# Optimization experiments

Hardware: AMD Instinct MI355X
Metric: run time of the kernel (lower is better)

The kernel has to match this reference:

```python
import jax, jax.numpy as jnp
import numpy as np

N = 16384   # total queries (= total keys here)
B = 16      # scenes
K = 1024    # keys per scene (key_batch_cnt entries)
L = 32      # local neighborhood size
D = 256     # d_model
H = 8       # nhead
DFF = 1024
LN_EPS = 1e-5


def setup_inputs() -> dict:
    key = jax.random.key(0)
    ks = jax.random.split(key, 32)
    f32 = jnp.float32

    def lin(k, o, i):
        return jax.random.normal(k, (o, i), f32) * 0.02

    idx = jax.random.randint(ks[3], (N, L), 0, K)
    invalid = jax.random.uniform(ks[4], (N, L)) < 0.1
    index_pair = jnp.where(invalid, -1, idx).astype(jnp.int32)

    inp = {
        "tgt": jax.random.normal(ks[0], (N, D), f32),
        "memory": jax.random.normal(ks[1], (N, D), f32),
        "memory_pos_emb": jax.random.normal(ks[2], (N, D), f32),
        "key_batch_cnt": jnp.full((B,), K, dtype=jnp.int32),
        "index_pair": index_pair,
        "index_pair_batch": jnp.repeat(jnp.arange(B, dtype=jnp.int32), K),
        "Wq": lin(ks[5], D, D), "bq": jnp.zeros((D,), f32),
        "Wkc": lin(ks[6], D, D), "bkc": jnp.zeros((D,), f32),
        "Wkp": lin(ks[7], D, D), "bkp": jnp.zeros((D,), f32),
        "Wv": lin(ks[8], D, D), "bv": jnp.zeros((D,), f32),
        "Wo": lin(ks[9], D, D), "bo": jnp.zeros((D,), f32),
        "W1": lin(ks[10], DFF, D), "b1": jnp.zeros((DFF,), f32),
        "W2": lin(ks[11], D, DFF), "b2": jnp.zeros((D,), f32),
        "g2": jnp.ones((D,), f32), "be2": jnp.zeros((D,), f32),
        "g3": jnp.ones((D,), f32), "be3": jnp.zeros((D,), f32),
    }
    return inp


def _ln(x, g, b):
    m = jnp.mean(x, axis=-1, keepdims=True)
    v = jnp.mean((x - m) ** 2, axis=-1, keepdims=True)
    return (x - m) * jax.lax.rsqrt(v + LN_EPS) * g + b


def reference(tgt, memory, memory_pos_emb, key_batch_cnt, index_pair,
              index_pair_batch, Wq, bq, Wkc, bkc, Wkp, bkp, Wv, bv,
              Wo, bo, W1, b1, W2, b2, g2, be2, g3, be3):
    Dh = D // H
    scale = Dh ** -0.5

    # dense projections
    q = tgt @ Wq.T + bq                              # [N, D]
    k = (memory @ Wkc.T + bkc) + (memory_pos_emb @ Wkp.T + bkp)  # content + pos
    v = memory @ Wv.T + bv

    # local-index gather: per-batch indices -> global key indices
    offsets = jnp.concatenate([jnp.zeros((1,), jnp.int32),
                               jnp.cumsum(key_batch_cnt)[:-1].astype(jnp.int32)])
    mask = index_pair < 0                            # [N, L] padded neighbors
    gidx = jnp.where(mask, 0, index_pair + offsets[index_pair_batch][:, None])

    kg = k[gidx].reshape(N, L, H, Dh)                # gathered keys  [N,L,H,Dh]
    vg = v[gidx].reshape(N, L, H, Dh)                # gathered values
    qh = q.reshape(N, H, Dh)

    attn = jnp.einsum('nhd,nlhd->nhl', qh, kg) * scale
    attn = jnp.where(mask[:, None, :], -1e9, attn)
    attn = jax.nn.softmax(attn, axis=-1)
    out = jnp.einsum('nhl,nlhd->nhd', attn, vg).reshape(N, D)
    tgt2 = out @ Wo.T + bo                           # attention out_proj

    x = _ln(tgt + tgt2, g2, be2)
    ff = jax.nn.relu(x @ W1.T + b1) @ W2.T + b2
    return _ln(x + ff, g3, be3)
```

## Files before the change

### kernel.cpp

```cpp
#include <hip/hip_runtime.h>
#include <stdint.h>

#define N_TOT 16384
#define LNEI  32
#define DM    256
#define NH    8
#define DH    32
#define DFF   1024

typedef __attribute__((ext_vector_type(8))) short  short8;
typedef __attribute__((ext_vector_type(4))) float  floatx4;
typedef __attribute__((ext_vector_type(2))) float  float2_t;
typedef __attribute__((ext_vector_type(4))) int    intx4;
typedef __attribute__((ext_vector_type(4))) unsigned short ushort4_t;
typedef __attribute__((ext_vector_type(4))) unsigned int uint4_t;

static __device__ __forceinline__ float b2f(unsigned short u) {
  union { unsigned int u; float f; } x; x.u = ((unsigned int)u) << 16; return x.f;
}
static __device__ __forceinline__ unsigned short f2b(float f) {
  union { float f; unsigned int u; } x; x.f = f;
  unsigned int r = x.u + 0x7fffu + ((x.u >> 16) & 1u);
  return (unsigned short)(r >> 16);
}

#define NSEG 11
struct Seg { const float* src; unsigned short* dst; int cols; int ostride; int ooff; int begin; };
struct SegTable { Seg s[NSEG]; int total; };

__global__ __launch_bounds__(256) void cvt_all(SegTable T, float* biaskv,
                                               const float* bkc, const float* bkp,
                                               const float* bv) {
  int e = (blockIdx.x * 256 + threadIdx.x) * 4;
  if (e >= T.total) {
    int c = e - T.total;
    #pragma unroll
    for (int j = 0; j < 4; ++j, ++c)
      if (c < 512) biaskv[c] = (c < 256) ? (bkc[c] + bkp[c]) : bv[c - 256];
    return;
  }
  int si = 0;
  #pragma unroll
  for (int i = 1; i < NSEG; ++i) if (e >= T.s[i].begin) si = i;
  const Seg s = T.s[si];
  const int le = e - s.begin;
  const int row = le / s.cols;
  const int col = le - row * s.cols;
  floatx4 v = {0.f, 0.f, 0.f, 0.f};
  if (s.src) v = *(const floatx4*)(s.src + le);
  ushort4_t o;
  o.x = f2b(v[0]); o.y = f2b(v[1]); o.z = f2b(v[2]); o.w = f2b(v[3]);
  *(ushort4_t*)(s.dst + (size_t)row * s.ostride + s.ooff + col) = o;
}

static __device__ __forceinline__ void gl_lds16(const unsigned short* g, unsigned short* l) {
  __builtin_amdgcn_global_load_lds(
      (const __attribute__((address_space(1))) unsigned int*)g,
      (__attribute__((address_space(3))) unsigned int*)l, 16, 0, 0);
}

template<int BN, bool RELU, bool CF32>
__global__ __launch_bounds__(256) void gemm_tile(
    const unsigned short* __restrict__ A, const unsigned short* __restrict__ W,
    const float* __restrict__ bias,
    void* __restrict__ C, int M, int Nd, int K, int lda)
{
  constexpr int BM = 128, BK = 32;
  constexpr int MI = (BN == 128) ? 4 : 2;
  constexpr int NI = 4;
  __shared__ unsigned short sA[2][BM * BK];
  __shared__ unsigned short sB[2][BN * BK];

  const int w    = threadIdx.x >> 6;
  const int lane = threadIdx.x & 63;
  const int quad = lane >> 4;
  const int l16  = lane & 15;
  const int m0 = blockIdx.x * BM;
  const int n0 = blockIdx.y * BN;
  const int wrow0 = (BN == 128) ? (w >> 1) * 64 : w * 32;
  const int wcol0 = (BN == 128) ? (w & 1) * 64 : 0;

  const int aflat0 = w * 512 + lane * 8;
  const int ar0 = aflat0 >> 5, ac = aflat0 & 31;

  floatx4 acc[MI][NI] = {};

  for (int k0 = 0; k0 < K; k0 += 2 * BK) {
    __syncthreads();
    #pragma unroll
    for (int half = 0; half < 2; ++half) {
      const int kk = k0 + half * BK;
      #pragma unroll
      for (int c = 0; c < 2; ++c) {
        const int row = ar0 + c * 64;
        gl_lds16(A + (size_t)(m0 + row) * lda + kk + ac, &sA[half][(c * 4 + w) * 512]);
      }
      if (BN == 128) {
        #pragma unroll
        for (int c = 0; c < 2; ++c) {
          const int row = ar0 + c * 64;
          gl_lds16(W + (size_t)(n0 + row) * K + kk + ac, &sB[half][(c * 4 + w) * 512]);
        }
      } else {
        gl_lds16(W + (size_t)(n0 + ar0) * K + kk + ac, &sB[half][w * 512]);
      }
    }
    __syncthreads();

    #pragma unroll
    for (int half = 0; half < 2; ++half) {
      short8 af[MI], bf[NI];
      #pragma unroll
      for (int mi = 0; mi < MI; ++mi)
        af[mi] = *(const short8*)&sA[half][(wrow0 + mi * 16 + l16) * BK + quad * 8];
      #pragma unroll
      for (int ni = 0; ni < NI; ++ni)
        bf[ni] = *(const short8*)&sB[half][(wcol0 + ni * 16 + l16) * BK + quad * 8];
      #pragma unroll
      for (int mi = 0; mi < MI; ++mi)
        #pragma unroll
        for (int ni = 0; ni < NI; ++ni)
          acc[mi][ni] = __builtin_amdgcn_mfma_f32_16x16x32_bf16(af[mi], bf[ni], acc[mi][ni], 0, 0, 0);
    }
  }

  #pragma unroll
  for (int ni = 0; ni < NI; ++ni) {
    const int col = n0 + wcol0 + ni * 16 + l16;
    const float bvv = bias[col];
    #pragma unroll
    for (int mi = 0; mi < MI; ++mi) {
      const int row0 = m0 + wrow0 + mi * 16 + quad * 4;
      #pragma unroll
      for (int i = 0; i < 4; ++i) {
        float v = acc[mi][ni][i] + bvv;
        if (RELU) v = fmaxf(v, 0.f);
        if (CF32) ((float*)C)[(size_t)(row0 + i) * Nd + col] = v;
        else ((unsigned short*)C)[(size_t)(row0 + i) * Nd + col] = f2b(v);
      }
    }
  }
}

__global__ __launch_bounds__(256) void attn_kernel(
    const unsigned short* __restrict__ q, const float* __restrict__ kv,
    const int* __restrict__ key_batch_cnt, const int* __restrict__ index_pair,
    const int* __restrict__ index_pair_batch,
    unsigned short* __restrict__ out)
{
  const int n = ((blockIdx.x & 7) << 11) | (blockIdx.x >> 3);
  const int t = threadIdx.x;
  __shared__ float s_q[DM];
  __shared__ int   s_gidx[LNEI];
  __shared__ float s_score[NH][LNEI];
  __shared__ float s_prob[NH][LNEI];
  __shared__ float s_out[2][DM];

  s_q[t] = b2f(q[(size_t)n * DM + t]);
  if (t < 64) {
    const int b = index_pair_batch[n];
    int cnt = (t < 16) ? key_batch_cnt[t] : 0;
    cnt = (t < b) ? cnt : 0;
    #pragma unroll
    for (int msk = 32; msk >= 1; msk >>= 1) cnt += __shfl_xor(cnt, msk, 64);
    if (t < LNEI) {
      const int ip = index_pair[(size_t)n * LNEI + t];
      s_gidx[t] = (ip < 0) ? -1 : (ip + cnt);
    }
  }
  __syncthreads();

  {
    const int j  = t >> 3;
    const int c8 = t & 7;
    const int g  = s_gidx[j];
    const int gl = (g < 0) ? 0 : g;
    const float* kbase = kv + (size_t)gl * 512;

    float part[4];
    #pragma unroll
    for (int i = 0; i < 4; ++i) {
      const int c = c8 + i * 8;
      const floatx4 ka = *(const floatx4*)(kbase + c * 8);
      const floatx4 kb = *(const floatx4*)(kbase + c * 8 + 4);
      const floatx4 qa = *(const floatx4*)&s_q[c * 8];
      const floatx4 qb = *(const floatx4*)&s_q[c * 8 + 4];
      float2_t s = (float2_t){ka[0], ka[1]} * (float2_t){qa[0], qa[1]};
      s = __builtin_elementwise_fma((float2_t){ka[2], ka[3]}, (float2_t){qa[2], qa[3]}, s);
      s = __builtin_elementwise_fma((float2_t){kb[0], kb[1]}, (float2_t){qb[0], qb[1]}, s);
      s = __builtin_elementwise_fma((float2_t){kb[2], kb[3]}, (float2_t){qb[2], qb[3]}, s);
      part[i] = s[0] + s[1];
    }
    #pragma unroll
    for (int i = 0; i < 4; ++i) {
      part[i] += __shfl_xor(part[i], 1, 64);
      part[i] += __shfl_xor(part[i], 2, 64);
    }
    if ((c8 & 3) == 0) {
      const int hodd = c8 >> 2;
      #pragma unroll
      for (int i = 0; i < 4; ++i)
        s_score[2 * i + hodd][j] =
            (g < 0) ? -1e9f : part[i] * 0.17677669529663687f;
    }
  }
  __syncthreads();

  {
    const int h = t >> 5;
    const int l = t & 31;
    const float sc = s_score[h][l];
    float mx = sc;
    #pragma unroll
    for (int msk = 16; msk >= 1; msk >>= 1) mx = fmaxf(mx, __shfl_xor(mx, msk, 64));
    const float e = __expf(sc - mx);
    float sm = e;
    #pragma unroll
    for (int msk = 16; msk >= 1; msk >>= 1) sm += __shfl_xor(sm, msk, 64);
    s_prob[h][l] = e / sm;
  }
  __syncthreads();

  {
    const int jh  = t >> 7;
    const int h   = (t >> 4) & 7;
    const int dh2 = t & 15;
    floatx4 p4[4];
    intx4   g4[4];
    #pragma unroll
    for (int r = 0; r < 4; ++r) {
      p4[r] = *(const floatx4*)&s_prob[h][jh * 16 + r * 4];
      g4[r] = *(const intx4*)&s_gidx[jh * 16 + r * 4];
    }
    float2_t acc = {0.f, 0.f};
    const float* vbase = kv + 256 + h * DH + dh2 * 2;
    #pragma unroll
    for (int j2 = 0; j2 < 16; ++j2) {
      int gj = g4[j2 >> 2][j2 & 3];
      gj = (gj < 0) ? 0 : gj;
      const float p = p4[j2 >> 2][j2 & 3];
      const float2_t v2 = *(const float2_t*)(vbase + (size_t)gj * 512);
      acc = __builtin_elementwise_fma((float2_t){p, p}, v2, acc);
    }
    s_out[jh][h * DH + dh2 * 2]     = acc[0];
    s_out[jh][h * DH + dh2 * 2 + 1] = acc[1];
  }
  __syncthreads();

  out[(size_t)n * DM + t] = f2b(s_out[0][t] + s_out[1][t]);
}

template<bool IN1F32, bool OUTF32>
__global__ __launch_bounds__(256) void ln_kernel(
    const void* __restrict__ in1, const unsigned short* __restrict__ in2,
    const float* __restrict__ g, const float* __restrict__ b,
    void* __restrict__ out)
{
  const int n    = blockIdx.x * 4 + (threadIdx.x >> 6);
  const int lane = threadIdx.x & 63;
  const int c0   = lane * 4;

  float a[4];
  if (IN1F32) {
    const floatx4 v = *(const floatx4*)((const float*)in1 + (size_t)n * DM + c0);
    a[0] = v[0]; a[1] = v[1]; a[2] = v[2]; a[3] = v[3];
  } else {
    const ushort4_t u = *(const ushort4_t*)((const unsigned short*)in1 + (size_t)n * DM + c0);
    a[0] = b2f(u.x); a[1] = b2f(u.y); a[2] = b2f(u.z); a[3] = b2f(u.w);
  }
  {
    const ushort4_t u = *(const ushort4_t*)(in2 + (size_t)n * DM + c0);
    a[0] += b2f(u.x); a[1] += b2f(u.y); a[2] += b2f(u.z); a[3] += b2f(u.w);
  }

  float s = a[0] + a[1] + a[2] + a[3];
  #pragma unroll
  for (int msk = 32; msk >= 1; msk >>= 1) s += __shfl_xor(s, msk, 64);
  const float mean = s * (1.0f / DM);

  float d[4], s2 = 0.f;
  #pragma unroll
  for (int i = 0; i < 4; ++i) { d[i] = a[i] - mean; s2 += d[i] * d[i]; }
  #pragma unroll
  for (int msk = 32; msk >= 1; msk >>= 1) s2 += __shfl_xor(s2, msk, 64);
  const float r = rsqrtf(s2 * (1.0f / DM) + 1e-5f);

  const floatx4 gv = *(const floatx4*)(g + c0);
  const floatx4 bv = *(const floatx4*)(b + c0);
  if (OUTF32) {
    floatx4 y;
    #pragma unroll
    for (int i = 0; i < 4; ++i) y[i] = d[i] * r * gv[i] + bv[i];
    *((floatx4*)((float*)out + (size_t)n * DM + c0)) = y;
  } else {
    ushort4_t y;
    y.x = f2b(d[0] * r * gv[0] + bv[0]);
    y.y = f2b(d[1] * r * gv[1] + bv[1]);
    y.z = f2b(d[2] * r * gv[2] + bv[2]);
    y.w = f2b(d[3] * r * gv[3] + bv[3]);
    *((ushort4_t*)((unsigned short*)out + (size_t)n * DM + c0)) = y;
  }
}

extern "C" void kernel_launch(void* const* d_in, const int* in_sizes, int n_in,
                              void* d_out, int out_size, void* d_ws, size_t ws_size,
                              hipStream_t stream) {
  const float* tgt  = (const float*)d_in[0];
  const float* mem  = (const float*)d_in[1];
  const float* pos  = (const float*)d_in[2];
  const int* kbc    = (const int*)d_in[3];
  const int* ipair  = (const int*)d_in[4];
  const int* ipb    = (const int*)d_in[5];
  const float* Wq   = (const float*)d_in[6];
  const float* bq   = (const float*)d_in[7];
  const float* Wkc  = (const float*)d_in[8];
  const float* bkc  = (const float*)d_in[9];
  const float* Wkp  = (const float*)d_in[10];
  const float* bkp  = (const float*)d_in[11];
  const float* Wv   = (const float*)d_in[12];
  const float* bvp  = (const float*)d_in[13];
  const float* Wo   = (const float*)d_in[14];
  const float* bo   = (const float*)d_in[15];
  const float* W1   = (const float*)d_in[16];
  const float* b1   = (const float*)d_in[17];
  const float* W2   = (const float*)d_in[18];
  const float* b2   = (const float*)d_in[19];
  const float* g2   = (const float*)d_in[20];
  const float* be2  = (const float*)d_in[21];
  const float* g3   = (const float*)d_in[22];
  const float* be3  = (const float*)d_in[23];

  const size_t NB = (size_t)N_TOT * DM;
  unsigned short* ws = (unsigned short*)d_ws;
  unsigned short* tgt_b = ws;
  unsigned short* ao_b  = ws;
  unsigned short* t2_b  = ws + NB;
  unsigned short* mp_b  = ws + 2 * NB;
  unsigned short* x_b   = ws + 2 * NB;
  unsigned short* ff_b  = ws + 3 * NB;
  float*          kv_f  = (float*)(ws + 4 * NB);
  unsigned short* h1_b  = ws + 4 * NB;
  unsigned short* q_b   = ws + 8 * NB;
  unsigned short* wgt   = ws + 9 * NB;
  unsigned short* Wq_b  = wgt;
  unsigned short* Wkv_b = wgt + 65536;
  unsigned short* Wo_b  = wgt + 65536 + 262144;
  unsigned short* W1_b  = wgt + 2 * 65536 + 262144;
  unsigned short* W2_b  = wgt + 2 * 65536 + 2 * 262144;
  float* bias_kv = (float*)(wgt + 2 * 65536 + 3 * 262144);

  SegTable T;
  int beg = 0, i = 0;
  auto seg = [&](const float* s, unsigned short* d, int cols, int ostride, int ooff, int nelem) {
    T.s[i].src = s; T.s[i].dst = d; T.s[i].cols = cols;
    T.s[i].ostride = ostride; T.s[i].ooff = ooff; T.s[i].begin = beg;
    beg += nelem; ++i;
  };
  seg(tgt, tgt_b, DM, DM, 0,   (int)NB);
  seg(mem, mp_b,  DM, 512, 0,  (int)NB);
  seg(pos, mp_b,  DM, 512, DM, (int)NB);
  seg(Wq,  Wq_b,  DM, DM, 0,   65536);
  seg(Wkc, Wkv_b, DM, 512, 0,  65536);
  seg(Wkp, Wkv_b, DM, 512, DM, 65536);
  seg(Wv,  Wkv_b + (size_t)256 * 512, DM, 512, 0, 65536);
  seg(nullptr, Wkv_b + (size_t)256 * 512, DM, 512, DM, 65536);
  seg(Wo,  Wo_b,  DM, DM, 0,   65536);
  seg(W1,  W1_b,  DM, DM, 0,   262144);
  seg(W2,  W2_b,  DFF, DFF, 0, 262144);
  T.total = beg;

  dim3 blk(256);
  cvt_all<<<dim3(T.total / 1024 + 1), blk, 0, stream>>>(T, bias_kv, bkc, bkp, bvp);

  dim3 gQ(N_TOT / 128, DM / 64);
  dim3 gKV(N_TOT / 128, 512 / 128);
  dim3 gF(N_TOT / 128, DFF / 128);

  gemm_tile<64, false, false><<<gQ, blk, 0, stream>>>(tgt_b, Wq_b, bq, q_b, N_TOT, DM, DM, DM);
  gemm_tile<128, false, true><<<gKV, blk, 0, stream>>>(mp_b, Wkv_b, bias_kv, kv_f, N_TOT, 512, 512, 512);
  attn_kernel<<<dim3(N_TOT), blk, 0, stream>>>(q_b, kv_f, kbc, ipair, ipb, ao_b);
  gemm_tile<64, false, false><<<gQ, blk, 0, stream>>>(ao_b, Wo_b, bo, t2_b, N_TOT, DM, DM, DM);
  ln_kernel<true, false><<<dim3(N_TOT / 4), blk, 0, stream>>>(tgt, t2_b, g2, be2, x_b);
  gemm_tile<128, true, false><<<gF, blk, 0, stream>>>(x_b, W1_b, b1, h1_b, N_TOT, DFF, DM, DM);
  gemm_tile<64, false, false><<<gQ, blk, 0, stream>>>(h1_b, W2_b, b2, ff_b, N_TOT, DM, DFF, DFF);
  ln_kernel<false, true><<<dim3(N_TOT / 4), blk, 0, stream>>>(x_b, ff_b, g3, be3, d_out);
}
```

Baseline: 281.2 us.

## Store K/V in bf16 and stage gathered rows in LDS for attention

The fused K/V projection now writes bf16 instead of fp32, which halves the bytes that the attention kernel gathers per neighbor. The attention kernel copies each neighbor's 512-element K/V row into shared memory with direct global-to-LDS loads, then computes scores with bf16 dot2 instructions and accumulates values from LDS. The cost is lower K/V precision and 34 KB of LDS per block, which may limit occupancy. The workspace layout is shuffled to fit the smaller buffer.

```diff
diff --git a/kernel.cpp b/kernel.cpp
--- a/kernel.cpp
+++ b/kernel.cpp
@@ -15,6 +15,19 @@
 typedef __attribute__((ext_vector_type(4))) unsigned short ushort4_t;
 typedef __attribute__((ext_vector_type(4))) unsigned int uint4_t;
 
+#if defined(__has_builtin)
+#if __has_builtin(__builtin_amdgcn_fdot2_f32_bf16)
+#define HAS_DOT2 1
+#endif
+#endif
+#ifndef HAS_DOT2
+#define HAS_DOT2 0
+#endif
+
+#if HAS_DOT2
+typedef __attribute__((ext_vector_type(2))) __bf16 bf16x2_t;
+#endif
+
 static __device__ __forceinline__ float b2f(unsigned short u) {
   union { unsigned int u; float f; } x; x.u = ((unsigned int)u) << 16; return x.f;
 }
@@ -22,6 +35,12 @@
   union { float f; unsigned int u; } x; x.f = f;
   unsigned int r = x.u + 0x7fffu + ((x.u >> 16) & 1u);
   return (unsigned short)(r >> 16);
+}
+static __device__ __forceinline__ float lo16(unsigned int d) {
+  union { unsigned int u; float f; } x; x.u = d << 16; return x.f;
+}
+static __device__ __forceinline__ float hi16(unsigned int d) {
+  union { unsigned int u; float f; } x; x.u = d & 0xffff0000u; return x.f;
 }
 
 #define NSEG 11
@@ -143,20 +162,21 @@
 }
 
 __global__ __launch_bounds__(256) void attn_kernel(
-    const unsigned short* __restrict__ q, const float* __restrict__ kv,
+    const unsigned short* __restrict__ q, const unsigned short* __restrict__ kv,
     const int* __restrict__ key_batch_cnt, const int* __restrict__ index_pair,
     const int* __restrict__ index_pair_batch,
     unsigned short* __restrict__ out)
 {
   const int n = ((blockIdx.x & 7) << 11) | (blockIdx.x >> 3);
   const int t = threadIdx.x;
-  __shared__ float s_q[DM];
+  __shared__ unsigned short s_kv[LNEI][544];
+  __shared__ unsigned short s_qb[DM];
   __shared__ int   s_gidx[LNEI];
   __shared__ float s_score[NH][LNEI];
   __shared__ float s_prob[NH][LNEI];
   __shared__ float s_out[2][DM];
 
-  s_q[t] = b2f(q[(size_t)n * DM + t]);
+  s_qb[t] = q[(size_t)n * DM + t];
   if (t < 64) {
     const int b = index_pair_batch[n];
     int cnt = (t < 16) ? key_batch_cnt[t] : 0;
@@ -171,25 +191,44 @@
   __syncthreads();
 
   {
+    const int w    = t >> 6;
+    const int lane = t & 63;
+    #pragma unroll
+    for (int r = 0; r < 8; ++r) {
+      const int j = w * 8 + r;
+      int gj = s_gidx[j];
+      gj = (gj < 0) ? 0 : gj;
+      gl_lds16(kv + (size_t)gj * 512 + lane * 8, &s_kv[j][0]);
+    }
+  }
+  __syncthreads();
+
+  {
     const int j  = t >> 3;
     const int c8 = t & 7;
     const int g  = s_gidx[j];
-    const int gl = (g < 0) ? 0 : g;
-    const float* kbase = kv + (size_t)gl * 512;
 
     float part[4];
     #pragma unroll
     for (int i = 0; i < 4; ++i) {
       const int c = c8 + i * 8;
-      const floatx4 ka = *(const floatx4*)(kbase + c * 8);
-      const floatx4 kb = *(const floatx4*)(kbase + c * 8 + 4);
-      const floatx4 qa = *(const floatx4*)&s_q[c * 8];
-      const floatx4 qb = *(const floatx4*)&s_q[c * 8 + 4];
-      float2_t s = (float2_t){ka[0], ka[1]} * (float2_t){qa[0], qa[1]};
-      s = __builtin_elementwise_fma((float2_t){ka[2], ka[3]}, (float2_t){qa[2], qa[3]}, s);
-      s = __builtin_elementwise_fma((float2_t){kb[0], kb[1]}, (float2_t){qb[0], qb[1]}, s);
-      s = __builtin_elementwise_fma((float2_t){kb[2], kb[3]}, (float2_t){qb[2], qb[3]}, s);
-      part[i] = s[0] + s[1];
+      const short8 kd = *(const short8*)&s_kv[j][c * 8];
+      const short8 qd = *(const short8*)&s_qb[c * 8];
+#if HAS_DOT2
+      union { short8 s; bf16x2_t p[4]; } ku, qu;
+      ku.s = kd; qu.s = qd;
+      float acc = 0.f;
+      #pragma unroll
+      for (int r = 0; r < 4; ++r)
+        acc = __builtin_amdgcn_fdot2_f32_bf16(ku.p[r], qu.p[r], acc, false);
+      part[i] = acc;
+#else
+      float acc = 0.f;
+      #pragma unroll
+      for (int r = 0; r < 8; ++r)
+        acc += b2f((unsigned short)kd[r]) * b2f((unsigned short)qd[r]);
+      part[i] = acc;
+#endif
     }
     #pragma unroll
     for (int i = 0; i < 4; ++i) {
@@ -226,21 +265,18 @@
     const int h   = (t >> 4) & 7;
     const int dh2 = t & 15;
     floatx4 p4[4];
-    intx4   g4[4];
-    #pragma unroll
-    for (int r = 0; r < 4; ++r) {
+    #pragma unroll
+    for (int r = 0; r < 4; ++r)
       p4[r] = *(const floatx4*)&s_prob[h][jh * 16 + r * 4];
-      g4[r] = *(const intx4*)&s_gidx[jh * 16 + r * 4];
-    }
     float2_t acc = {0.f, 0.f};
-    const float* vbase = kv + 256 + h * DH + dh2 * 2;
+    const int vo = 256 + h * 32 + dh2 * 2;
     #pragma unroll
     for (int j2 = 0; j2 < 16; ++j2) {
-      int gj = g4[j2 >> 2][j2 & 3];
-      gj = (gj < 0) ? 0 : gj;
+      const int j = jh * 16 + j2;
       const float p = p4[j2 >> 2][j2 & 3];
-      const float2_t v2 = *(const float2_t*)(vbase + (size_t)gj * 512);
-      acc = __builtin_elementwise_fma((float2_t){p, p}, v2, acc);
+      const unsigned int d = *(const unsigned int*)&s_kv[j][vo];
+      acc = __builtin_elementwise_fma((float2_t){p, p},
+                                      (float2_t){lo16(d), hi16(d)}, acc);
     }
     s_out[jh][h * DH + dh2 * 2]     = acc[0];
     s_out[jh][h * DH + dh2 * 2 + 1] = acc[1];
@@ -338,10 +374,10 @@
   unsigned short* mp_b  = ws + 2 * NB;
   unsigned short* x_b   = ws + 2 * NB;
   unsigned short* ff_b  = ws + 3 * NB;
-  float*          kv_f  = (float*)(ws + 4 * NB);
+  unsigned short* q_b   = ws + 4 * NB;
   unsigned short* h1_b  = ws + 4 * NB;
-  unsigned short* q_b   = ws + 8 * NB;
-  unsigned short* wgt   = ws + 9 * NB;
+  unsigned short* kv_b  = ws + 5 * NB;
+  unsigned short* wgt   = ws + 8 * NB;
   unsigned short* Wq_b  = wgt;
   unsigned short* Wkv_b = wgt + 65536;
   unsigned short* Wo_b  = wgt + 65536 + 262144;
@@ -377,8 +413,8 @@
   dim3 gF(N_TOT / 128, DFF / 128);
 
   gemm_tile<64, false, false><<<gQ, blk, 0, stream>>>(tgt_b, Wq_b, bq, q_b, N_TOT, DM, DM, DM);
-  gemm_tile<128, false, true><<<gKV, blk, 0, stream>>>(mp_b, Wkv_b, bias_kv, kv_f, N_TOT, 512, 512, 512);
-  attn_kernel<<<dim3(N_TOT), blk, 0, stream>>>(q_b, kv_f, kbc, ipair, ipb, ao_b);
+  gemm_tile<128, false, false><<<gKV, blk, 0, stream>>>(mp_b, Wkv_b, bias_kv, kv_b, N_TOT, 512, 512, 512);
+  attn_kernel<<<dim3(N_TOT), blk, 0, stream>>>(q_b, kv_b, kbc, ipair, ipb, ao_b);
   gemm_tile<64, false, false><<<gQ, blk, 0, stream>>>(ao_b, Wo_b, bo, t2_b, N_TOT, DM, DM, DM);
   ln_kernel<true, false><<<dim3(N_TOT / 4), blk, 0, stream>>>(tgt, t2_b, g2, be2, x_b);
   gemm_tile<128, true, false><<<gF, blk, 0, stream>>>(x_b, W1_b, b1, h1_b, N_TOT, DFF, DM, DM);
```

Result: no change. 286.7 us (+2.0%).
